# Kernel tuning notes

Measured on AMD Instinct MI355X. Metric: run time of the kernel, lower is better.

The kernel has to match this reference:

```python
import jax, jax.numpy as jnp
import numpy as np

NEG = -1e9  # finite stand-in for -inf so downstream grads stay finite
NUM_HEADS = 16


def phm_linear(x, A, S, b):
    # PHM weight: W = sum_i kron(A[i], S[i]) -> (n*kin, n*kout)
    n, kin, kout = S.shape
    W = jnp.einsum('nab,nkl->akbl', A, S).reshape(n * kin, n * kout)
    return x @ W + b


def layer_norm(x, g, b, eps=1e-5):
    mu = jnp.mean(x, axis=-1, keepdims=True)
    var = jnp.var(x, axis=-1, keepdims=True)
    return (x - mu) / jnp.sqrt(var + eps) * g + b


def masking(V, lens):
    # DAG transition mask: vertex i may transition to j>i with j < len[b].
    i = jnp.arange(V)
    tri = i[None, :] > i[:, None]                       # (V,V) j > i
    valid = i[None, None, :] < lens[:, None, None]      # (B,1,V)
    m = tri[None, :, :] & valid
    dead = ~m.any(-1)                                   # (B,V) rows with no valid successor
    eye = jnp.eye(V, dtype=bool)
    m = m | (dead[:, :, None] & eye[None])              # keep softmax finite on dead rows
    return m, dead


def setup_inputs() -> dict:
    key = jax.random.key(0)
    ks = jax.random.split(key, 8)
    B, V, E, VOC = 8, 512, 1024, 32000
    s = 0.02
    return {
        'x': jax.random.normal(ks[0], (B, V, E), jnp.float32),
        'vertex_lens': jax.random.randint(ks[1], (B,), V // 2, V + 1),
        'ln_g': jnp.ones((E,), jnp.float32),
        'ln_b': jnp.zeros((E,), jnp.float32),
        'attn_A': jax.random.normal(ks[2], (4, 4, 4), jnp.float32) * 0.5,
        'attn_S': jax.random.normal(ks[3], (4, 256, 512), jnp.float32) * s,
        'attn_b': jnp.zeros((2 * E,), jnp.float32),
        'gate_A': jax.random.normal(ks[4], (4, 4, 4), jnp.float32) * 0.5,
        'gate_S': jax.random.normal(ks[5], (4, 256, 4), jnp.float32) * s,
        'gate_b': jnp.zeros((NUM_HEADS,), jnp.float32),
        'lm_A': jax.random.normal(ks[6], (2, 2, 2), jnp.float32) * 0.5,
        'lm_S': jax.random.normal(ks[7], (2, 512, 16000), jnp.float32) * s,
        'lm_b': jnp.zeros((VOC,), jnp.float32),
    }


def reference(x, vertex_lens, ln_g, ln_b, attn_A, attn_S, attn_b,
              gate_A, gate_S, gate_b, lm_A, lm_S, lm_b):
    B, V, E = x.shape
    H = NUM_HEADS
    cs = E // H
    xn = layer_norm(x, ln_g, ln_b)
    m, r = masking(V, vertex_lens)
    # gate over heads (B,V,H)
    g = jax.nn.log_softmax(phm_linear(xn, gate_A, gate_S, gate_b), axis=-1)
    qk = phm_linear(xn, attn_A, attn_S, attn_b)
    q, k = jnp.split(qk, 2, axis=-1)
    q = q.reshape(B, V, H, cs)
    k = k.reshape(B, V, H, cs)
    scores = jnp.einsum('bihf,bjhf->bijh', q, k) / jnp.asarray(np.sqrt(cs), jnp.float32)
    scores = jnp.where(m[..., None], scores, NEG)
    scores = jax.nn.log_softmax(scores, axis=2)          # normalize over successors j
    scores = jnp.where(r[:, :, None, None], NEG, scores)  # kill rows past length
    transition_matrix = jax.nn.logsumexp(scores + g[:, :, None, :], axis=-1)  # (B,V,V)
    vocab_log_probs = jax.nn.log_softmax(phm_linear(xn, lm_A, lm_S, lm_b), axis=-1)
    return transition_matrix, vocab_log_probs
```

## Files before the change

kernel.cpp:

```cpp
#include <hip/hip_runtime.h>
#include <hip/hip_bf16.h>
#include <hip/hip_fp8.h>
#include <stdint.h>

typedef __bf16 bf16x8 __attribute__((ext_vector_type(8)));
typedef __bf16 bf16x4 __attribute__((ext_vector_type(4)));
typedef float  f32x4  __attribute__((ext_vector_type(4)));
typedef int    i32x4  __attribute__((ext_vector_type(4)));
typedef int    i32x8  __attribute__((ext_vector_type(8)));

typedef __attribute__((address_space(3))) unsigned int as3_uint;
typedef const __attribute__((address_space(1))) unsigned int as1_uint;

#define NEGC (-1e9f)

__device__ __forceinline__ void async16(void* ldsPtr, const void* gPtr) {
    __builtin_amdgcn_global_load_lds((as1_uint*)(uintptr_t)gPtr,
                                     (as3_uint*)(uintptr_t)ldsPtr, 16, 0, 0);
}

__global__ __launch_bounds__(256) void ln_kernel(const float* __restrict__ x,
                                                 const float* __restrict__ gw,
                                                 const float* __restrict__ bw,
                                                 __bf16* __restrict__ xn,
                                                 unsigned char* __restrict__ xn8) {
    __shared__ float red[8];
    size_t row = blockIdx.x;
    int t = threadIdx.x;
    const float4* xr = (const float4*)(x + row * 1024);
    float4 v = xr[t];
    float s  = v.x + v.y + v.z + v.w;
    float ss = v.x*v.x + v.y*v.y + v.z*v.z + v.w*v.w;
    #pragma unroll
    for (int o = 32; o; o >>= 1) { s += __shfl_xor(s, o); ss += __shfl_xor(ss, o); }
    int wave = t >> 6, lane = t & 63;
    if (lane == 0) { red[wave*2] = s; red[wave*2+1] = ss; }
    __syncthreads();
    float S  = red[0] + red[2] + red[4] + red[6];
    float SS = red[1] + red[3] + red[5] + red[7];
    float mu  = S * (1.0f/1024.0f);
    float var = SS * (1.0f/1024.0f) - mu*mu;
    float rs  = rsqrtf(var + 1e-5f);
    float4 gv = ((const float4*)gw)[t];
    float4 bv = ((const float4*)bw)[t];
    float f0 = (v.x-mu)*rs*gv.x + bv.x;
    float f1 = (v.y-mu)*rs*gv.y + bv.y;
    float f2 = (v.z-mu)*rs*gv.z + bv.z;
    float f3 = (v.w-mu)*rs*gv.w + bv.w;
    bf16x4 o4;
    o4[0] = (__bf16)f0; o4[1] = (__bf16)f1; o4[2] = (__bf16)f2; o4[3] = (__bf16)f3;
    ((bf16x4*)(xn + row*1024))[t] = o4;
    unsigned int pk = (unsigned)__hip_fp8_e4m3(f0).__x
                    | ((unsigned)__hip_fp8_e4m3(f1).__x << 8)
                    | ((unsigned)__hip_fp8_e4m3(f2).__x << 16)
                    | ((unsigned)__hip_fp8_e4m3(f3).__x << 24);
    ((unsigned int*)(xn8 + row*1024))[t] = pk;
}

template<int OUT>
__global__ __launch_bounds__(256) void phm_build(const float* __restrict__ A,
                                                 const float* __restrict__ S,
                                                 void* __restrict__ Wt,
                                                 int nn, int kin, int kout) {
    __shared__ float sh[4][32][65];
    __shared__ float shA[64];
    int t  = threadIdx.x;
    int l0 = blockIdx.x * 64;
    int k0 = blockIdx.y * 32;
    int kt = nn * kin;
    if (t < nn*nn*nn) shA[t] = A[t];
    for (int n = 0; n < nn; ++n) {
        #pragma unroll
        for (int i = 0; i < 8; ++i) {
            int e = t + i*256;
            int kk = e >> 6, ll = e & 63;
            sh[n][kk][ll] = S[((size_t)(n*kin) + k0 + kk)*kout + l0 + ll];
        }
    }
    __syncthreads();
    for (int a = 0; a < nn; ++a)
        for (int b = 0; b < nn; ++b) {
            #pragma unroll
            for (int i = 0; i < 8; ++i) {
                int e = t + i*256;
                int kk = e & 31, ll = e >> 5;
                float val = 0.f;
                for (int n = 0; n < nn; ++n)
                    val += shA[(n*nn + a)*nn + b] * sh[n][kk][ll];
                size_t idx = (size_t)(b*kout + l0 + ll)*kt + a*kin + k0 + kk;
                if (OUT == 0) ((__bf16*)Wt)[idx] = (__bf16)val;
                else          ((unsigned char*)Wt)[idx] = __hip_fp8_e4m3(val * 16.0f).__x;
            }
        }
}

__global__ __launch_bounds__(256) void gatew_kernel(const float* __restrict__ A,
                                                    const float* __restrict__ S,
                                                    float* __restrict__ W) {
    int idx = blockIdx.x*256 + threadIdx.x;
    int r = idx >> 4, c = idx & 15;
    int a = r >> 8, k = r & 255, b = c >> 2, l = c & 3;
    float v = 0.f;
    #pragma unroll
    for (int n = 0; n < 4; ++n)
        v += A[(n*4 + a)*4 + b] * S[((size_t)(n*256 + k))*4 + l];
    W[idx] = v;
}

__global__ __launch_bounds__(256) void gemm_bt(const __bf16* __restrict__ A,
                                               const __bf16* __restrict__ Bt,
                                               const float* __restrict__ bias,
                                               float* __restrict__ C,
                                               int M, int N, int K) {
    __shared__ __align__(16) __bf16 As[128*64];
    __shared__ __align__(16) __bf16 Bs[128*64];
    int tid  = threadIdx.x;
    int wave = tid >> 6, lane = tid & 63;
    int m0 = blockIdx.y * 128, n0 = blockIdx.x * 128;
    int wm = (wave >> 1) * 64, wn = (wave & 1) * 64;
    int lrow = lane & 15, lk = lane >> 4;
    f32x4 acc[4][4] = {};
    for (int k0 = 0; k0 < K; k0 += 64) {
        #pragma unroll
        for (int q = 0; q < 4; ++q) {
            int o   = q*4096 + tid*16;
            int row = o >> 7;
            int sp  = (o >> 4) & 7;
            int s   = sp ^ (row & 7);
            async16((char*)As + q*4096 + wave*1024,
                    (const char*)A  + ((size_t)(m0+row)*K + k0 + s*8)*2);
            async16((char*)Bs + q*4096 + wave*1024,
                    (const char*)Bt + ((size_t)(n0+row)*K + k0 + s*8)*2);
        }
        __syncthreads();
        #pragma unroll
        for (int kk = 0; kk < 2; ++kk) {
            bf16x8 af[4], bfr[4];
            #pragma unroll
            for (int mi = 0; mi < 4; ++mi) {
                int r = wm + mi*16 + lrow;
                int off = r*128 + ((kk*64 + lk*16) ^ ((r & 7) << 4));
                af[mi] = *(const bf16x8*)((const char*)As + off);
            }
            #pragma unroll
            for (int ni = 0; ni < 4; ++ni) {
                int r = wn + ni*16 + lrow;
                int off = r*128 + ((kk*64 + lk*16) ^ ((r & 7) << 4));
                bfr[ni] = *(const bf16x8*)((const char*)Bs + off);
            }
            #pragma unroll
            for (int mi = 0; mi < 4; ++mi)
                #pragma unroll
                for (int ni = 0; ni < 4; ++ni)
                    acc[mi][ni] = __builtin_amdgcn_mfma_f32_16x16x32_bf16(
                        af[mi], bfr[ni], acc[mi][ni], 0, 0, 0);
        }
        __syncthreads();
    }
    #pragma unroll
    for (int ni = 0; ni < 4; ++ni) {
        int col = n0 + wn + ni*16 + lrow;
        float bv = bias ? bias[col] : 0.f;
        #pragma unroll
        for (int mi = 0; mi < 4; ++mi) {
            #pragma unroll
            for (int r = 0; r < 4; ++r) {
                int rowg = m0 + wm + mi*16 + lk*4 + r;
                C[(size_t)rowg*N + col] = acc[mi][ni][r] + bv;
            }
        }
    }
}

__global__ __launch_bounds__(256) void gemm_mx_lm(const unsigned char* __restrict__ A8,
                                                  const unsigned char* __restrict__ B8,
                                                  const float* __restrict__ bias,
                                                  void* __restrict__ Cv) {
    const int K = 1024, N = 32000;
    __shared__ __align__(16) unsigned char As[128*128];
    __shared__ __align__(16) unsigned char Bs[128*128];
    int tid = threadIdx.x;
    int wave = tid >> 6, lane = tid & 63;
    int bid  = blockIdx.x;
    int wg   = (bid & 7) * 1000 + (bid >> 3);
    int band = wg / 2000;
    int rem  = wg % 2000;
    int nt   = rem >> 3;
    int mt   = band * 8 + (rem & 7);
    int m0 = mt * 128, n0 = nt * 128;
    int wm = (wave >> 1) * 64, wn = (wave & 1) * 64;
    int lrow = lane & 15, lk = lane >> 4;
    f32x4 acc[4][4] = {};
    for (int k0 = 0; k0 < K; k0 += 128) {
        #pragma unroll
        for (int q = 0; q < 4; ++q) {
            int o = q*4096 + tid*16;
            int r = o >> 7;
            int p = (o >> 4) & 7;
            int g = p ^ (r & 7);
            async16((char*)As + q*4096 + wave*1024,
                    (const char*)A8 + (size_t)(m0+r)*K + k0 + g*16);
            async16((char*)Bs + q*4096 + wave*1024,
                    (const char*)B8 + (size_t)(n0+r)*K + k0 + g*16);
        }
        __syncthreads();
        i32x8 af[4], bfr[4];
        #pragma unroll
        for (int mi = 0; mi < 4; ++mi) {
            int r = wm + mi*16 + lrow;
            int c0 = lk*2;
            i32x4 lo = *(const i32x4*)(As + r*128 + ((c0    ^ (r&7))*16));
            i32x4 hi = *(const i32x4*)(As + r*128 + (((c0+1) ^ (r&7))*16));
            af[mi] = __builtin_shufflevector(lo, hi, 0,1,2,3,4,5,6,7);
        }
        #pragma unroll
        for (int ni = 0; ni < 4; ++ni) {
            int r = wn + ni*16 + lrow;
            int c0 = lk*2;
            i32x4 lo = *(const i32x4*)(Bs + r*128 + ((c0    ^ (r&7))*16));
            i32x4 hi = *(const i32x4*)(Bs + r*128 + (((c0+1) ^ (r&7))*16));
            bfr[ni] = __builtin_shufflevector(lo, hi, 0,1,2,3,4,5,6,7);
        }
        #pragma unroll
        for (int mi = 0; mi < 4; ++mi)
            #pragma unroll
            for (int ni = 0; ni < 4; ++ni)
                acc[mi][ni] = __builtin_amdgcn_mfma_scale_f32_16x16x128_f8f6f4(
                    af[mi], bfr[ni], acc[mi][ni],
                    0 , 0 , 0, 127, 0, 127);
        __syncthreads();
    }
    #pragma unroll
    for (int ni = 0; ni < 4; ++ni) {
        int col = n0 + wn + ni*16 + lrow;
        float bv = bias ? bias[col] : 0.f;
        #pragma unroll
        for (int mi = 0; mi < 4; ++mi) {
            #pragma unroll
            for (int r = 0; r < 4; ++r) {
                int rowg = m0 + wm + mi*16 + lk*4 + r;
                float val = acc[mi][ni][r] * 0.0625f + bv;
                ((__bf16*)((char*)Cv + (size_t)rowg * N * 4))[col] = (__bf16)val;
            }
        }
    }
}

__global__ __launch_bounds__(256) void gate_kernel(const __bf16* __restrict__ xn,
                                                   const float* __restrict__ Wg,
                                                   const float* __restrict__ gb,
                                                   float* __restrict__ Gp) {
    __shared__ float xr[16][65];
    __shared__ float red[16][17];
    size_t row = blockIdx.x;
    int t = threadIdx.x;
    bf16x4 v = ((const bf16x4*)(xn + row*1024))[t];
    #pragma unroll
    for (int q = 0; q < 4; ++q) {
        int e = t*4 + q;
        xr[e >> 6][e & 63] = (float)v[q];
    }
    __syncthreads();
    int h = t & 15, sl = t >> 4;
    float p = 0.f;
    #pragma unroll
    for (int u = 0; u < 64; ++u) p += xr[sl][u] * Wg[(sl*64 + u)*16 + h];
    red[sl][h] = p;
    __syncthreads();
    if (t < 16) {
        float logit = gb[t];
        #pragma unroll
        for (int s2 = 0; s2 < 16; ++s2) logit += red[s2][t];
        float m = logit;
        #pragma unroll
        for (int o = 8; o; o >>= 1) m = fmaxf(m, __shfl_xor(m, o, 16));
        float e = __expf(logit - m);
        float ssum = e;
        #pragma unroll
        for (int o = 8; o; o >>= 1) ssum += __shfl_xor(ssum, o, 16);
        Gp[row*16 + t] = e / ssum;
    }
}

__global__ __launch_bounds__(256) void scores_kernel(const float* __restrict__ qk,
                                                     const float* __restrict__ Gp,
                                                     const int* __restrict__ lens,
                                                     float* __restrict__ out) {
    __shared__ float qs[8][1024];
    __shared__ float gps[8][16];
    __shared__ float wredB[2][4][8];
    int bid = blockIdx.x;
    int b   = bid & 7;
    int i0  = (bid >> 3) * 8;
    int t   = threadIdx.x;
    int wave = t >> 6, lane = t & 63;
    int len = lens[b];
    const float4* qbase = (const float4*)(qk + ((size_t)b*512 + i0)*2048);
    #pragma unroll
    for (int s = 0; s < 8; ++s) {
        int e = t + s*256;
        int ti = e >> 8, c4 = e & 255;
        ((float4*)qs)[e] = qbase[ti*512 + c4];
    }
    if (t < 128) gps[t >> 4][t & 15] = Gp[((size_t)b*512 + i0 + (t >> 4))*16 + (t & 15)];
    __syncthreads();
    int j0 = t, j1 = t + 256;
    const float4* kp0 = (const float4*)(qk + ((size_t)b*512 + j0)*2048 + 1024);
    const float4* kp1 = (const float4*)(qk + ((size_t)b*512 + j1)*2048 + 1024);
    float acc0[8] = {}, acc1[8] = {}, mace[8] = {};
    for (int h = 0; h < 16; ++h) {
        float4 kv0[16], kv1[16];
        #pragma unroll
        for (int u = 0; u < 16; ++u) { kv0[u] = kp0[h*16 + u]; kv1[u] = kp1[h*16 + u]; }
        float pex0[8], pex1[8];
        #pragma unroll
        for (int ti = 0; ti < 8; ++ti) {
            const float* qrow = &qs[ti][h*64];
            float d0 = 0.f, d1 = 0.f;
            #pragma unroll
            for (int u = 0; u < 16; ++u) {
                float q0 = qrow[u*4+0], q1 = qrow[u*4+1], q2 = qrow[u*4+2], q3 = qrow[u*4+3];
                d0 += kv0[u].x*q0 + kv0[u].y*q1 + kv0[u].z*q2 + kv0[u].w*q3;
                d1 += kv1[u].x*q0 + kv1[u].y*q1 + kv1[u].z*q2 + kv1[u].w*q3;
            }
            int i = i0 + ti;
            float sc0 = (j0 > i && j0 < len) ? d0 * 0.125f : NEGC;
            float sc1 = (j1 > i && j1 < len) ? d1 * 0.125f : NEGC;
            float pe0 = __expf(sc0), pe1 = __expf(sc1);
            pex0[ti] = pe0; pex1[ti] = pe1;
            float vv = pe0 + pe1;
            #pragma unroll
            for (int o = 32; o; o >>= 1) vv += __shfl_xor(vv, o);
            if (lane == 0) wredB[h & 1][wave][ti] = vv;
        }
        __syncthreads();
        #pragma unroll
        for (int ti = 0; ti < 8; ++ti) {
            float gs = wredB[h & 1][0][ti] + wredB[h & 1][1][ti]
                     + wredB[h & 1][2][ti] + wredB[h & 1][3][ti];
            float inv = 1.0f / gs;
            float g = gps[ti][h];
            acc0[ti] += pex0[ti] * inv * g;
            acc1[ti] += pex1[ti] * inv * g;
            mace[ti] += g * inv;
        }
    }
    #pragma unroll
    for (int ti = 0; ti < 8; ++ti) {
        int i = i0 + ti;
        float lm = NEGC + __logf(mace[ti]);
        float v0, v1;
        if (i >= len - 1) { v0 = NEGC; v1 = NEGC; }
        else {
            v0 = (j0 > i && j0 < len) ? __logf(acc0[ti]) : lm;
            v1 = (j1 > i && j1 < len) ? __logf(acc1[ti]) : lm;
        }
        out[((size_t)b*512 + i)*512 + j0] = v0;
        out[((size_t)b*512 + i)*512 + j1] = v1;
    }
}

__global__ __launch_bounds__(256) void vocab_softmax_bf16(float* __restrict__ out) {
    __shared__ float red[8];
    size_t row = blockIdx.x;
    char* rowbase = (char*)out + row * (size_t)32000 * 4;
    const bf16x8* g8 = (const bf16x8*)rowbase;
    int t = threadIdx.x, wave = t >> 6, lane = t & 63;
    bf16x8 cc[16];
    float mx = -1e30f;
    #pragma unroll
    for (int s = 0; s < 16; ++s) {
        int v = t + s*256;
        if (v < 4000) {
            cc[s] = g8[v];
            #pragma unroll
            for (int jj = 0; jj < 8; ++jj) mx = fmaxf(mx, (float)cc[s][jj]);
        }
    }
    #pragma unroll
    for (int o = 32; o; o >>= 1) mx = fmaxf(mx, __shfl_xor(mx, o));
    if (lane == 0) red[wave] = mx;
    __syncthreads();
    mx = fmaxf(fmaxf(red[0], red[1]), fmaxf(red[2], red[3]));
    float sum = 0.f;
    #pragma unroll
    for (int s = 0; s < 16; ++s) {
        int v = t + s*256;
        if (v < 4000) {
            #pragma unroll
            for (int jj = 0; jj < 8; ++jj) sum += __expf((float)cc[s][jj] - mx);
        }
    }
    #pragma unroll
    for (int o = 32; o; o >>= 1) sum += __shfl_xor(sum, o);
    if (lane == 0) red[4 + wave] = sum;
    __syncthreads();
    float lse = mx + __logf(red[4] + red[5] + red[6] + red[7]);
    float4* o4 = (float4*)rowbase;
    #pragma unroll
    for (int s = 0; s < 16; ++s) {
        int v = t + s*256;
        if (v < 4000) {
            float4 a, b;
            a.x = (float)cc[s][0] - lse; a.y = (float)cc[s][1] - lse;
            a.z = (float)cc[s][2] - lse; a.w = (float)cc[s][3] - lse;
            b.x = (float)cc[s][4] - lse; b.y = (float)cc[s][5] - lse;
            b.z = (float)cc[s][6] - lse; b.w = (float)cc[s][7] - lse;
            o4[v*2]   = a;
            o4[v*2+1] = b;
        }
    }
}

extern "C" void kernel_launch(void* const* d_in, const int* in_sizes, int n_in,
                              void* d_out, int out_size, void* d_ws, size_t ws_size,
                              hipStream_t stream) {
    (void)in_sizes; (void)n_in; (void)out_size; (void)ws_size;
    const float* x      = (const float*)d_in[0];
    const int*   lens   = (const int*)  d_in[1];
    const float* ln_g   = (const float*)d_in[2];
    const float* ln_b   = (const float*)d_in[3];
    const float* attn_A = (const float*)d_in[4];
    const float* attn_S = (const float*)d_in[5];
    const float* attn_b = (const float*)d_in[6];
    const float* gate_A = (const float*)d_in[7];
    const float* gate_S = (const float*)d_in[8];
    const float* gate_b = (const float*)d_in[9];
    const float* lm_A   = (const float*)d_in[10];
    const float* lm_S   = (const float*)d_in[11];
    const float* lm_b   = (const float*)d_in[12];

    float* out_trans = (float*)d_out;
    float* out_vocab = out_trans + (size_t)8*512*512;

    char* ws = (char*)d_ws;
    __bf16*        xn     = (__bf16*)(ws);
    unsigned char* xn8    = (unsigned char*)(ws + 8388608);
    __bf16*        WtAttn = (__bf16*)(ws + 12582912);
    unsigned char* WtLm8  = (unsigned char*)(ws + 16777216);
    float*         Wg     = (float*)(ws + 49545216);
    float*         qkbuf  = (float*)(ws + 49610752);
    float*         Gp     = (float*)(ws + 83165184);

    hipLaunchKernelGGL(ln_kernel,    dim3(4096),     dim3(256), 0, stream, x, ln_g, ln_b, xn, xn8);
    hipLaunchKernelGGL(gatew_kernel, dim3(64),       dim3(256), 0, stream, gate_A, gate_S, Wg);
    hipLaunchKernelGGL((phm_build<0>), dim3(8, 8),   dim3(256), 0, stream, attn_A, attn_S, (void*)WtAttn, 4, 256, 512);
    hipLaunchKernelGGL((phm_build<1>), dim3(250, 16),dim3(256), 0, stream, lm_A, lm_S, (void*)WtLm8, 2, 512, 16000);
    hipLaunchKernelGGL(gemm_bt,      dim3(16, 32),   dim3(256), 0, stream,
                       xn, WtAttn, attn_b, qkbuf, 4096, 2048, 1024);
    hipLaunchKernelGGL(gate_kernel,  dim3(4096),     dim3(256), 0, stream, xn, Wg, gate_b, Gp);
    hipLaunchKernelGGL(scores_kernel,dim3(512),      dim3(256), 0, stream, qkbuf, Gp, lens, out_trans);
    hipLaunchKernelGGL(gemm_mx_lm,   dim3(8000),     dim3(256), 0, stream,
                       xn8, WtLm8, lm_b, (void*)out_vocab);
    hipLaunchKernelGGL(vocab_softmax_bf16, dim3(4096), dim3(256), 0, stream, out_vocab);
}
```

Measured before the change: 694.3 us.

## Use FP8 MX GEMM for QK projection and restructure scores kernel

Switches the attention QK projection from a bf16 MFMA GEMM to the templated FP8 scaled MFMA GEMM shared with the LM head, building the attention PHM weight in FP8. The scores kernel now uses 512 threads per block, each owning one column j over 16 query rows. Q slices are double-buffered per head in shared memory instead of staging full 8x1024 rows, and waves whose columns are fully masked skip their dot products. This cuts GEMM cost and scores-kernel work and register pressure, at the risk of FP8 precision loss in the attention scores.

```diff
diff --git a/kernel.cpp b/kernel.cpp
--- a/kernel.cpp
+++ b/kernel.cpp
@@ -107,87 +107,27 @@
     W[idx] = v;
 }
 
-__global__ __launch_bounds__(256) void gemm_bt(const __bf16* __restrict__ A,
-                                               const __bf16* __restrict__ Bt,
+template<int SWZ, int OUTMODE>
+__global__ __launch_bounds__(256) void gemm_mx(const unsigned char* __restrict__ A8,
+                                               const unsigned char* __restrict__ B8,
                                                const float* __restrict__ bias,
-                                               float* __restrict__ C,
-                                               int M, int N, int K) {
-    __shared__ __align__(16) __bf16 As[128*64];
-    __shared__ __align__(16) __bf16 Bs[128*64];
-    int tid  = threadIdx.x;
-    int wave = tid >> 6, lane = tid & 63;
-    int m0 = blockIdx.y * 128, n0 = blockIdx.x * 128;
-    int wm = (wave >> 1) * 64, wn = (wave & 1) * 64;
-    int lrow = lane & 15, lk = lane >> 4;
-    f32x4 acc[4][4] = {};
-    for (int k0 = 0; k0 < K; k0 += 64) {
-        #pragma unroll
-        for (int q = 0; q < 4; ++q) {
-            int o   = q*4096 + tid*16;
-            int row = o >> 7;
-            int sp  = (o >> 4) & 7;
-            int s   = sp ^ (row & 7);
-            async16((char*)As + q*4096 + wave*1024,
-                    (const char*)A  + ((size_t)(m0+row)*K + k0 + s*8)*2);
-            async16((char*)Bs + q*4096 + wave*1024,
-                    (const char*)Bt + ((size_t)(n0+row)*K + k0 + s*8)*2);
-        }
-        __syncthreads();
-        #pragma unroll
-        for (int kk = 0; kk < 2; ++kk) {
-            bf16x8 af[4], bfr[4];
-            #pragma unroll
-            for (int mi = 0; mi < 4; ++mi) {
-                int r = wm + mi*16 + lrow;
-                int off = r*128 + ((kk*64 + lk*16) ^ ((r & 7) << 4));
-                af[mi] = *(const bf16x8*)((const char*)As + off);
-            }
-            #pragma unroll
-            for (int ni = 0; ni < 4; ++ni) {
-                int r = wn + ni*16 + lrow;
-                int off = r*128 + ((kk*64 + lk*16) ^ ((r & 7) << 4));
-                bfr[ni] = *(const bf16x8*)((const char*)Bs + off);
-            }
-            #pragma unroll
-            for (int mi = 0; mi < 4; ++mi)
-                #pragma unroll
-                for (int ni = 0; ni < 4; ++ni)
-                    acc[mi][ni] = __builtin_amdgcn_mfma_f32_16x16x32_bf16(
-                        af[mi], bfr[ni], acc[mi][ni], 0, 0, 0);
-        }
-        __syncthreads();
-    }
-    #pragma unroll
-    for (int ni = 0; ni < 4; ++ni) {
-        int col = n0 + wn + ni*16 + lrow;
-        float bv = bias ? bias[col] : 0.f;
-        #pragma unroll
-        for (int mi = 0; mi < 4; ++mi) {
-            #pragma unroll
-            for (int r = 0; r < 4; ++r) {
-                int rowg = m0 + wm + mi*16 + lk*4 + r;
-                C[(size_t)rowg*N + col] = acc[mi][ni][r] + bv;
-            }
-        }
-    }
-}
-
-__global__ __launch_bounds__(256) void gemm_mx_lm(const unsigned char* __restrict__ A8,
-                                                  const unsigned char* __restrict__ B8,
-                                                  const float* __restrict__ bias,
-                                                  void* __restrict__ Cv) {
-    const int K = 1024, N = 32000;
+                                               void* __restrict__ Cv,
+                                               int N, int K) {
     __shared__ __align__(16) unsigned char As[128*128];
     __shared__ __align__(16) unsigned char Bs[128*128];
     int tid = threadIdx.x;
     int wave = tid >> 6, lane = tid & 63;
-    int bid  = blockIdx.x;
-    int wg   = (bid & 7) * 1000 + (bid >> 3);
-    int band = wg / 2000;
-    int rem  = wg % 2000;
-    int nt   = rem >> 3;
-    int mt   = band * 8 + (rem & 7);
-    int m0 = mt * 128, n0 = nt * 128;
+    int m0, n0;
+    if (SWZ) {
+        int bid  = blockIdx.x;
+        int wg   = (bid & 7) * 1000 + (bid >> 3);
+        int band = wg / 2000;
+        int rem  = wg % 2000;
+        m0 = (band * 8 + (rem & 7)) * 128;
+        n0 = (rem >> 3) * 128;
+    } else {
+        m0 = blockIdx.y * 128; n0 = blockIdx.x * 128;
+    }
     int wm = (wave >> 1) * 64, wn = (wave & 1) * 64;
     int lrow = lane & 15, lk = lane >> 4;
     f32x4 acc[4][4] = {};
@@ -240,7 +180,10 @@
             for (int r = 0; r < 4; ++r) {
                 int rowg = m0 + wm + mi*16 + lk*4 + r;
                 float val = acc[mi][ni][r] * 0.0625f + bv;
-                ((__bf16*)((char*)Cv + (size_t)rowg * N * 4))[col] = (__bf16)val;
+                if (OUTMODE == 1)
+                    ((__bf16*)((char*)Cv + (size_t)rowg * N * 4))[col] = (__bf16)val;
+                else
+                    ((float*)Cv)[(size_t)rowg * N + col] = val;
             }
         }
     }
@@ -282,81 +225,88 @@
     }
 }
 
-__global__ __launch_bounds__(256) void scores_kernel(const float* __restrict__ qk,
+__global__ __launch_bounds__(512) void scores_kernel(const float* __restrict__ qk,
                                                      const float* __restrict__ Gp,
                                                      const int* __restrict__ lens,
                                                      float* __restrict__ out) {
-    __shared__ float qs[8][1024];
-    __shared__ float gps[8][16];
-    __shared__ float wredB[2][4][8];
+    __shared__ __align__(16) float qsh[2][16][64];
+    __shared__ float gps[16][16];
+    __shared__ float wredB[2][8][16];
     int bid = blockIdx.x;
     int b   = bid & 7;
-    int i0  = (bid >> 3) * 8;
+    int i0  = (bid >> 3) * 16;
     int t   = threadIdx.x;
     int wave = t >> 6, lane = t & 63;
     int len = lens[b];
-    const float4* qbase = (const float4*)(qk + ((size_t)b*512 + i0)*2048);
-    #pragma unroll
-    for (int s = 0; s < 8; ++s) {
-        int e = t + s*256;
-        int ti = e >> 8, c4 = e & 255;
-        ((float4*)qs)[e] = qbase[ti*512 + c4];
-    }
-    if (t < 128) gps[t >> 4][t & 15] = Gp[((size_t)b*512 + i0 + (t >> 4))*16 + (t & 15)];
-    __syncthreads();
-    int j0 = t, j1 = t + 256;
-    const float4* kp0 = (const float4*)(qk + ((size_t)b*512 + j0)*2048 + 1024);
-    const float4* kp1 = (const float4*)(qk + ((size_t)b*512 + j1)*2048 + 1024);
-    float acc0[8] = {}, acc1[8] = {}, mace[8] = {};
+    if (t < 256) {
+        int ti = t >> 4;
+        gps[ti][t & 15] = Gp[((size_t)b*512 + i0 + ti)*16 + (t & 15)];
+        int u = t & 15;
+        ((float4*)qsh[0][ti])[u] =
+            *(const float4*)(qk + ((size_t)b*512 + i0 + ti)*2048 + u*4);
+    }
+    int j = t;
+    const float4* kp = (const float4*)(qk + ((size_t)b*512 + j)*2048 + 1024);
+    bool wlive = ((wave*64 + 63) > i0) && (wave*64 < len);
+    float acc[16] = {}, mace[16] = {};
+    __syncthreads();
     for (int h = 0; h < 16; ++h) {
-        float4 kv0[16], kv1[16];
-        #pragma unroll
-        for (int u = 0; u < 16; ++u) { kv0[u] = kp0[h*16 + u]; kv1[u] = kp1[h*16 + u]; }
-        float pex0[8], pex1[8];
-        #pragma unroll
-        for (int ti = 0; ti < 8; ++ti) {
-            const float* qrow = &qs[ti][h*64];
-            float d0 = 0.f, d1 = 0.f;
-            #pragma unroll
-            for (int u = 0; u < 16; ++u) {
-                float q0 = qrow[u*4+0], q1 = qrow[u*4+1], q2 = qrow[u*4+2], q3 = qrow[u*4+3];
-                d0 += kv0[u].x*q0 + kv0[u].y*q1 + kv0[u].z*q2 + kv0[u].w*q3;
-                d1 += kv1[u].x*q0 + kv1[u].y*q1 + kv1[u].z*q2 + kv1[u].w*q3;
+        int cur = h & 1;
+        if (h + 1 < 16 && t < 256) {
+            int ti = t >> 4, u = t & 15;
+            ((float4*)qsh[cur^1][ti])[u] =
+                *(const float4*)(qk + ((size_t)b*512 + i0 + ti)*2048 + (h+1)*64 + u*4);
+        }
+        float pex[16];
+        if (wlive) {
+            float4 kv[16];
+            #pragma unroll
+            for (int u = 0; u < 16; ++u) kv[u] = kp[h*16 + u];
+            #pragma unroll
+            for (int ti = 0; ti < 16; ++ti) {
+                const float* qrow = qsh[cur][ti];
+                float d = 0.f;
+                #pragma unroll
+                for (int u = 0; u < 16; ++u)
+                    d += kv[u].x*qrow[u*4+0] + kv[u].y*qrow[u*4+1]
+                       + kv[u].z*qrow[u*4+2] + kv[u].w*qrow[u*4+3];
+                int i = i0 + ti;
+                float sc = (j > i && j < len) ? d * 0.125f : NEGC;
+                float pe = __expf(sc);
+                pex[ti] = pe;
+                float vv = pe;
+                #pragma unroll
+                for (int o = 32; o; o >>= 1) vv += __shfl_xor(vv, o);
+                if (lane == 0) wredB[cur][wave][ti] = vv;
             }
-            int i = i0 + ti;
-            float sc0 = (j0 > i && j0 < len) ? d0 * 0.125f : NEGC;
-            float sc1 = (j1 > i && j1 < len) ? d1 * 0.125f : NEGC;
-            float pe0 = __expf(sc0), pe1 = __expf(sc1);
-            pex0[ti] = pe0; pex1[ti] = pe1;
-            float vv = pe0 + pe1;
-            #pragma unroll
-            for (int o = 32; o; o >>= 1) vv += __shfl_xor(vv, o);
-            if (lane == 0) wredB[h & 1][wave][ti] = vv;
+        } else {
+            #pragma unroll
+            for (int ti = 0; ti < 16; ++ti) pex[ti] = 0.f;
+            if (lane == 0) {
+                #pragma unroll
+                for (int ti = 0; ti < 16; ++ti) wredB[cur][wave][ti] = 0.f;
+            }
         }
         __syncthreads();
         #pragma unroll
-        for (int ti = 0; ti < 8; ++ti) {
-            float gs = wredB[h & 1][0][ti] + wredB[h & 1][1][ti]
-                     + wredB[h & 1][2][ti] + wredB[h & 1][3][ti];
+        for (int ti = 0; ti < 16; ++ti) {
+            float gs = 0.f;
+            #pragma unroll
+            for (int w = 0; w < 8; ++w) gs += wredB[cur][w][ti];
             float inv = 1.0f / gs;
             float g = gps[ti][h];
-            acc0[ti] += pex0[ti] * inv * g;
-            acc1[ti] += pex1[ti] * inv * g;
+            acc[ti]  += pex[ti] * inv * g;
             mace[ti] += g * inv;
         }
     }
     #pragma unroll
-    for (int ti = 0; ti < 8; ++ti) {
+    for (int ti = 0; ti < 16; ++ti) {
         int i = i0 + ti;
-        float lm = NEGC + __logf(mace[ti]);
-        float v0, v1;
-        if (i >= len - 1) { v0 = NEGC; v1 = NEGC; }
-        else {
-            v0 = (j0 > i && j0 < len) ? __logf(acc0[ti]) : lm;
-            v1 = (j1 > i && j1 < len) ? __logf(acc1[ti]) : lm;
-        }
-        out[((size_t)b*512 + i)*512 + j0] = v0;
-        out[((size_t)b*512 + i)*512 + j1] = v1;
+        float val;
+        if (i >= len - 1)            val = NEGC;
+        else if (j > i && j < len)   val = __logf(acc[ti]);
+        else                         val = NEGC + __logf(mace[ti]);
+        out[((size_t)b*512 + i)*512 + j] = val;
     }
 }
 
@@ -434,23 +384,23 @@
     float* out_vocab = out_trans + (size_t)8*512*512;
 
     char* ws = (char*)d_ws;
-    __bf16*        xn     = (__bf16*)(ws);
-    unsigned char* xn8    = (unsigned char*)(ws + 8388608);
-    __bf16*        WtAttn = (__bf16*)(ws + 12582912);
-    unsigned char* WtLm8  = (unsigned char*)(ws + 16777216);
-    float*         Wg     = (float*)(ws + 49545216);
-    float*         qkbuf  = (float*)(ws + 49610752);
-    float*         Gp     = (float*)(ws + 83165184);
+    __bf16*        xn      = (__bf16*)(ws);
+    unsigned char* xn8     = (unsigned char*)(ws + 8388608);
+    unsigned char* WtAttn8 = (unsigned char*)(ws + 12582912);
+    unsigned char* WtLm8   = (unsigned char*)(ws + 14680064);
+    float*         Wg      = (float*)(ws + 47448064);
+    float*         qkbuf   = (float*)(ws + 47513600);
+    float*         Gp      = (float*)(ws + 81068032);
 
     hipLaunchKernelGGL(ln_kernel,    dim3(4096),     dim3(256), 0, stream, x, ln_g, ln_b, xn, xn8);
     hipLaunchKernelGGL(gatew_kernel, dim3(64),       dim3(256), 0, stream, gate_A, gate_S, Wg);
-    hipLaunchKernelGGL((phm_build<0>), dim3(8, 8),   dim3(256), 0, stream, attn_A, attn_S, (void*)WtAttn, 4, 256, 512);
+    hipLaunchKernelGGL((phm_build<1>), dim3(8, 8),   dim3(256), 0, stream, attn_A, attn_S, (void*)WtAttn8, 4, 256, 512);
     hipLaunchKernelGGL((phm_build<1>), dim3(250, 16),dim3(256), 0, stream, lm_A, lm_S, (void*)WtLm8, 2, 512, 16000);
-    hipLaunchKernelGGL(gemm_bt,      dim3(16, 32),   dim3(256), 0, stream,
-                       xn, WtAttn, attn_b, qkbuf, 4096, 2048, 1024);
+    hipLaunchKernelGGL((gemm_mx<0,0>), dim3(16, 32), dim3(256), 0, stream,
+                       xn8, WtAttn8, attn_b, (void*)qkbuf, 2048, 1024);
     hipLaunchKernelGGL(gate_kernel,  dim3(4096),     dim3(256), 0, stream, xn, Wg, gate_b, Gp);
-    hipLaunchKernelGGL(scores_kernel,dim3(512),      dim3(256), 0, stream, qkbuf, Gp, lens, out_trans);
-    hipLaunchKernelGGL(gemm_mx_lm,   dim3(8000),     dim3(256), 0, stream,
-                       xn8, WtLm8, lm_b, (void*)out_vocab);
+    hipLaunchKernelGGL(scores_kernel,dim3(256),      dim3(512), 0, stream, qkbuf, Gp, lens, out_trans);
+    hipLaunchKernelGGL((gemm_mx<1,1>), dim3(8000),   dim3(256), 0, stream,
+                       xn8, WtLm8, lm_b, (void*)out_vocab, 32000, 1024);
     hipLaunchKernelGGL(vocab_softmax_bf16, dim3(4096), dim3(256), 0, stream, out_vocab);
 }
```

Result: slower. 714.4 us (+2.9%).
